# Kernel optimization log

Hardware: AMD Instinct MI355X
Metric: run time of the kernel (lower is better)

## Reference

```python
import jax, jax.numpy as jnp
import numpy as np

# Model config (matches init_kwargs)
DAG_DEPTH = 16
HIDDEN = 2048
B, T = 4, 4096
N = DAG_DEPTH                 # total_nodes
INIT_SLOTS = DAG_DEPTH // 2   # initial slots
INTER = DAG_DEPTH // 2        # intermediate slots / scan steps
LOG_CLAMP = 23.026
SIGN_TEMP = 1e-4


def _xavier(k, shape):
    fan_out, fan_in = shape
    lim = np.sqrt(6.0 / (fan_in + fan_out)).astype(np.float32)
    return jax.random.uniform(k, shape, jnp.float32, -lim, lim)


def setup_inputs() -> dict:
    key = jax.random.key(0)
    k0, k1, k2, k3 = jax.random.split(key, 4)
    return {
        "hidden": jax.random.normal(k0, (B, T, HIDDEN), jnp.float32),
        "W_init": _xavier(k1, (2 * N, HIDDEN)),
        "b_init": jnp.zeros((2 * N,), jnp.float32),
        "W_op": _xavier(k2, (INTER * N, HIDDEN)),
        "b_op": jnp.zeros((INTER * N,), jnp.float32),
        "W_gate": _xavier(k3, (INTER, HIDDEN)),
        "b_gate": jnp.zeros((INTER,), jnp.float32),
    }


def reference(hidden, W_init, b_init, W_op, b_op, W_gate, b_gate):
    Bb, Tt, H = hidden.shape
    # --- plan predictor ---
    init_raw = jnp.einsum('bth,oh->bto', hidden, W_init) + b_init        # (B,T,2N)
    V_mag = jnp.abs(init_raw[..., :N])                                   # (B,T,N)
    V_sign = jnp.tanh(init_raw[..., N:])                                 # (B,T,N)
    O = (jnp.einsum('bth,oh->bto', hidden, W_op) + b_op).reshape(Bb, Tt, INTER, N)
    G = jax.nn.sigmoid(jnp.einsum('bth,oh->bto', hidden, W_gate) + b_gate)  # (B,T,INTER)

    # --- sequential DAG execution (fixed INTER steps, vectorized over B,T) ---
    # NOTE: torch casts to float64 (float32 on mps); here we compute in float32,
    # identical math modulo precision (jax x64 is disabled by default).
    pos = jnp.arange(N)
    for step in range(INTER):
        valid = INIT_SLOTS + step
        mask = (pos < valid).astype(hidden.dtype)                        # causal mask over nodes
        O_s = O[:, :, step, :] * mask                                    # (B,T,N)
        G_s = G[:, :, step:step + 1]                                     # (B,T,1)
        signed = V_sign * V_mag
        log_mag = jnp.log(jnp.clip(V_mag, 1e-12))
        mixed = log_mag * (1.0 - G_s) + signed * G_s
        R = jnp.sum(O_s * mixed, axis=-1, keepdims=True)                 # (B,T,1)
        lin_sign = jnp.tanh(R / SIGN_TEMP)
        sign_prod = jnp.prod(V_sign * (jnp.abs(O_s) + 1.0), axis=-1, keepdims=True)
        log_sign = jnp.tanh(sign_prod / SIGN_TEMP)
        Vs_new = G_s * lin_sign + (1.0 - G_s) * log_sign
        Vm_new = G_s * jnp.abs(R) + (1.0 - G_s) * jnp.exp(jnp.clip(R, None, LOG_CLAMP))
        idx = INIT_SLOTS + step
        V_mag = V_mag.at[:, :, idx].set(Vm_new[..., 0])
        V_sign = V_sign.at[:, :, idx].set(Vs_new[..., 0])

    return V_sign[:, :, -1] * V_mag[:, :, -1]                            # (B,T)
```

## Files before the change

### kernel.cpp

```cpp
#include <hip/hip_runtime.h>
#include <math.h>

#define HID    2048
#define NROW   16384
#define NCOL   168
#define BM     64
#define KSTEPS 64
#define NSUP   32
#define NELEM  2112
#define SLICE  33792
#define SUPB   67584
#define CPD    172
#define NSLOT  16
#define NSTEP  8

typedef short short8 __attribute__((ext_vector_type(8)));
typedef float f32x4  __attribute__((ext_vector_type(4)));
typedef unsigned int u32x4 __attribute__((ext_vector_type(4)));

static __device__ __forceinline__ void wait_vm8() {
  asm volatile("s_waitcnt vmcnt(8)" ::: "memory");
}

static __device__ __forceinline__ unsigned pack_hi(unsigned u0, unsigned u1) {
  return __builtin_amdgcn_perm(u1, u0, 0x07060302u);
}

struct Planes { u32x4 p1, p2, p3; };
static __device__ __forceinline__ Planes split8(const float* x) {
  Planes P;
  #pragma unroll
  for (int q = 0; q < 4; ++q) {
    float x0 = x[2*q], x1 = x[2*q+1];
    unsigned u0 = __float_as_uint(x0), u1 = __float_as_uint(x1);
    P.p1[q] = pack_hi(u0, u1);
    float r0 = x0 - __uint_as_float(u0 & 0xFFFF0000u);
    float r1 = x1 - __uint_as_float(u1 & 0xFFFF0000u);
    unsigned v0 = __float_as_uint(r0), v1 = __float_as_uint(r1);
    P.p2[q] = pack_hi(v0, v1);
    float s0 = r0 - __uint_as_float(v0 & 0xFFFF0000u);
    float s1 = r1 - __uint_as_float(v1 & 0xFFFF0000u);
    P.p3[q] = pack_hi(__float_as_uint(s0), __float_as_uint(s1));
  }
  return P;
}

static __device__ __forceinline__ void loadA8(const float* p, float* x) {
  f32x4 a = *(const f32x4*)p;
  f32x4 b = *(const f32x4*)(p + 4);
  x[0]=a[0]; x[1]=a[1]; x[2]=a[2]; x[3]=a[3];
  x[4]=b[0]; x[5]=b[1]; x[6]=b[2]; x[7]=b[3];
}

static __device__ __forceinline__ f32x4 mf(short8 a, short8 b, f32x4 c) {
  return __builtin_amdgcn_mfma_f32_16x16x32_bf16(a, b, c, 0, 0, 0);
}

static __device__ __forceinline__ void gld_lds16(const void* g, void* l) {
  __builtin_amdgcn_global_load_lds(
      (const __attribute__((address_space(1))) unsigned int*)g,
      (__attribute__((address_space(3))) unsigned int*)l, 16, 0, 0);
}

__global__ void prep_b(const float* __restrict__ Wi, const float* __restrict__ Wo,
                       const float* __restrict__ Wg, u32x4* __restrict__ wsB) {
  int bid  = blockIdx.x;
  int kidx = bid / 11;
  int nt   = bid - kidx * 11;
  int l    = threadIdx.x;
  int col  = nt * 16 + (l & 15);
  int k0   = kidx * 32 + (l >> 4) * 8;

  float x[8];
  if (col < NCOL) {
    const float* wr = (col < 32)  ? (Wi + (size_t)col * HID)
                    : (col < 160) ? (Wo + (size_t)(col - 32) * HID)
                                  : (Wg + (size_t)(col - 160) * HID);
    loadA8(wr + k0, x);
  } else {
    #pragma unroll
    for (int i = 0; i < 8; ++i) x[i] = 0.f;
  }
  Planes P = split8(x);
  size_t base = (size_t)kidx * NELEM + (nt * 3) * 64 + l;
  wsB[base]       = P.p1;
  wsB[base + 64]  = P.p2;
  wsB[base + 128] = P.p3;
}

__global__ __launch_bounds__(512, 2)
void dag_main(const float* __restrict__ hidden, const u32x4* __restrict__ wsB,
              const float* __restrict__ b_init, const float* __restrict__ b_op,
              const float* __restrict__ b_gate, float* __restrict__ out)
{
  __shared__ __align__(16) char smem[2 * SUPB];

  const int tid = threadIdx.x;
  const int l   = tid & 63;
  const int w   = tid >> 6;
  const int wn  = w & 3;
  const int wm  = w >> 2;
  const int row0 = blockIdx.x * BM;
  const int r   = l & 15;
  const int kg  = l >> 4;

  const float* ap0 = hidden + (size_t)(row0 + wm * 32 + r) * HID + kg * 8;
  const float* ap1 = ap0 + (size_t)16 * HID;

  const int cb = 9 * wn + (wm ? ((wn == 3) ? 1 : 4) : 0);
  const u32x4* gsrc[5];
  char* ldst[5];
  #pragma unroll
  for (int i = 0; i < 5; ++i) {
    gsrc[i] = wsB + (size_t)(cb + i) * 64 + l;
    ldst[i] = smem + (cb + i) * 1024;
  }
  const char* brd0 = smem + (size_t)(9 * wn) * 1024 + (size_t)l * 16;

  f32x4 acc[2][3];
  const f32x4 zf = {0.f, 0.f, 0.f, 0.f};
  #pragma unroll
  for (int mt = 0; mt < 2; ++mt)
    #pragma unroll
    for (int j = 0; j < 3; ++j) acc[mt][j] = zf;

  float xe0[8], xe1[8], xo0[8], xo1[8];

#define STAGE(s_, sel_) do {                                                 \
    _Pragma("unroll")                                                        \
    for (int q = 0; q < 2; ++q)                                              \
      _Pragma("unroll")                                                      \
      for (int i = 0; i < 5; ++i)                                            \
        gld_lds16(gsrc[i] + (size_t)NELEM * (2 * (s_) + q),                  \
                  ldst[i] + (sel_) * SUPB + q * SLICE);                      \
  } while (0)

#define KSTEP(bb_, xc0_, xc1_, ISSA_, t2_) do {                              \
    short8 bf[9];                                                            \
    _Pragma("unroll")                                                        \
    for (int i = 0; i < 9; ++i)                                              \
      if (wn != 3 || i < 6) bf[i] = *(const short8*)((bb_) + i * 1024);      \
    Planes PA0 = split8(xc0_);                                               \
    Planes PA1 = split8(xc1_);                                               \
    if (ISSA_) {                                                             \
      loadA8(ap0 + (t2_) * 32, xc0_);                                        \
      loadA8(ap1 + (t2_) * 32, xc1_);                                        \
    }                                                                        \
    short8 a0p1 = __builtin_bit_cast(short8, PA0.p1);                        \
    short8 a0p2 = __builtin_bit_cast(short8, PA0.p2);                        \
    short8 a0p3 = __builtin_bit_cast(short8, PA0.p3);                        \
    short8 a1p1 = __builtin_bit_cast(short8, PA1.p1);                        \
    short8 a1p2 = __builtin_bit_cast(short8, PA1.p2);                        \
    short8 a1p3 = __builtin_bit_cast(short8, PA1.p3);                        \
    __builtin_amdgcn_s_setprio(1);                                           \
    _Pragma("unroll")                                                        \
    for (int j = 0; j < 3; ++j) {                                            \
      if (wn == 3 && j == 2) continue;                                       \
      short8 b1 = bf[j * 3 + 0];                                             \
      short8 b2 = bf[j * 3 + 1];                                             \
      short8 b3 = bf[j * 3 + 2];                                             \
      {                                                                      \
        f32x4 c = acc[0][j];                                                 \
        c = mf(a0p1, b1, c); c = mf(a0p1, b2, c); c = mf(a0p2, b1, c);       \
        c = mf(a0p1, b3, c); c = mf(a0p2, b2, c); c = mf(a0p3, b1, c);       \
        acc[0][j] = c;                                                       \
      }                                                                      \
      {                                                                      \
        f32x4 c = acc[1][j];                                                 \
        c = mf(a1p1, b1, c); c = mf(a1p1, b2, c); c = mf(a1p2, b1, c);       \
        c = mf(a1p1, b3, c); c = mf(a1p2, b2, c); c = mf(a1p3, b1, c);       \
        acc[1][j] = c;                                                       \
      }                                                                      \
    }                                                                        \
    __builtin_amdgcn_s_setprio(0);                                           \
  } while (0)

#define BODY(s_, p_, ISSUE_) do {                                            \
    wait_vm8();                                                              \
    __builtin_amdgcn_sched_barrier(0);                                       \
    __builtin_amdgcn_s_barrier();                                            \
    __builtin_amdgcn_sched_barrier(0);                                       \
    if (ISSUE_) STAGE((s_) + 1, (p_) ^ 1);                                   \
    const char* be = brd0 + (p_) * SUPB;                                     \
    KSTEP(be,         xe0, xe1, (ISSUE_), 2 * (s_) + 2);                     \
    KSTEP(be + SLICE, xo0, xo1, (ISSUE_), 2 * (s_) + 3);                     \
  } while (0)

  STAGE(0, 0);
  loadA8(ap0,      xe0);
  loadA8(ap1,      xe1);
  loadA8(ap0 + 32, xo0);
  loadA8(ap1 + 32, xo1);

  for (int s = 0; s < 30; s += 2) {
    BODY(s,     0, true);
    BODY(s + 1, 1, true);
  }
  BODY(30, 0, true);
  BODY(31, 1, false);
#undef BODY
#undef KSTEP
#undef STAGE

  __syncthreads();
  float (*sC)[CPD] = (float(*)[CPD])smem;
  #pragma unroll
  for (int mt = 0; mt < 2; ++mt) {
    #pragma unroll
    for (int j = 0; j < 3; ++j) {
      int col = wn * 48 + j * 16 + r;
      if (col < NCOL) {
        int row = wm * 32 + mt * 16 + kg * 4;
        sC[row + 0][col] = acc[mt][j][0];
        sC[row + 1][col] = acc[mt][j][1];
        sC[row + 2][col] = acc[mt][j][2];
        sC[row + 3][col] = acc[mt][j][3];
      }
    }
  }
  __syncthreads();

  if (tid < BM) {
    const int rr = tid;
    float Vm[NSLOT], Vs[NSLOT];
    #pragma unroll
    for (int i = 0; i < NSLOT; ++i) {
      float mv = sC[rr][i]      + b_init[i];
      float sv = sC[rr][16 + i] + b_init[16 + i];
      Vm[i] = fabsf(mv);
      Vs[i] = tanhf(sv);
    }
    float G[NSTEP];
    #pragma unroll
    for (int s = 0; s < NSTEP; ++s) {
      float gr = sC[rr][160 + s] + b_gate[s];
      G[s] = 1.0f / (1.0f + expf(-gr));
    }
    #pragma unroll
    for (int s = 0; s < NSTEP; ++s) {
      const float g = G[s];
      float R = 0.f, sp = 1.f;
      #pragma unroll
      for (int i = 0; i < NSLOT; ++i) {
        float Osi = (i < 8 + s) ? (sC[rr][32 + s * 16 + i] + b_op[s * 16 + i]) : 0.f;
        float sgn   = Vs[i] * Vm[i];
        float logm  = logf(fmaxf(Vm[i], 1e-12f));
        float mixed = logm * (1.f - g) + sgn * g;
        R  += Osi * mixed;
        sp *= Vs[i] * (fabsf(Osi) + 1.f);
      }
      float lin_sign = tanhf(R  / 1e-4f);
      float log_sign = tanhf(sp / 1e-4f);
      float vs_new = g * lin_sign + (1.f - g) * log_sign;
      float vm_new = g * fabsf(R) + (1.f - g) * expf(fminf(R, 23.026f));
      Vm[8 + s] = vm_new;
      Vs[8 + s] = vs_new;
    }
    out[row0 + rr] = Vs[NSLOT - 1] * Vm[NSLOT - 1];
  }
}

extern "C" void kernel_launch(void* const* d_in, const int* in_sizes, int n_in,
                              void* d_out, int out_size, void* d_ws, size_t ws_size,
                              hipStream_t stream) {
  (void)in_sizes; (void)n_in; (void)out_size; (void)ws_size;
  const float* hidden = (const float*)d_in[0];
  const float* W_init = (const float*)d_in[1];
  const float* b_init = (const float*)d_in[2];
  const float* W_op   = (const float*)d_in[3];
  const float* b_op   = (const float*)d_in[4];
  const float* W_gate = (const float*)d_in[5];
  const float* b_gate = (const float*)d_in[6];
  float* out = (float*)d_out;
  u32x4* wsB = (u32x4*)d_ws;

  prep_b<<<dim3(704), dim3(64), 0, stream>>>(W_init, W_op, W_gate, wsB);
  dag_main<<<dim3(NROW / BM), dim3(512), 0, stream>>>(hidden, wsB, b_init, b_op,
                                                      b_gate, out);
}
```

Before: 100.5 us.

## Split GEMM warp tiles to 16 rows per wave with 1024-thread blocks

Doubles the block to 16 waves, so each wave computes a 16-row by 48-column tile instead of 32 rows. The staging of B into LDS is redistributed across the four row-groups of waves, with 2-3 chunks each, and the vmcnt wait threshold is lowered to match the fewer loads per thread. The goal is more waves in flight to hide latency and lower register pressure per wave. Each B fragment read from LDS is now reused for only one A tile, so LDS read traffic doubles per MFMA, and occupancy drops to one block per CU.

```diff
diff --git a/kernel.cpp b/kernel.cpp
--- a/kernel.cpp
+++ b/kernel.cpp
@@ -6,7 +6,6 @@
 #define NCOL   168
 #define BM     64
 #define KSTEPS 64
-#define NSUP   32
 #define NELEM  2112
 #define SLICE  33792
 #define SUPB   67584
@@ -18,8 +17,8 @@
 typedef float f32x4  __attribute__((ext_vector_type(4)));
 typedef unsigned int u32x4 __attribute__((ext_vector_type(4)));
 
-static __device__ __forceinline__ void wait_vm8() {
-  asm volatile("s_waitcnt vmcnt(8)" ::: "memory");
+static __device__ __forceinline__ void wait_vm4() {
+  asm volatile("s_waitcnt vmcnt(4)" ::: "memory");
 }
 
 static __device__ __forceinline__ unsigned pack_hi(unsigned u0, unsigned u1) {
@@ -88,7 +87,7 @@
   wsB[base + 128] = P.p3;
 }
 
-__global__ __launch_bounds__(512, 2)
+__global__ __launch_bounds__(1024, 1)
 void dag_main(const float* __restrict__ hidden, const u32x4* __restrict__ wsB,
               const float* __restrict__ b_init, const float* __restrict__ b_op,
               const float* __restrict__ b_gate, float* __restrict__ out)
@@ -104,93 +103,74 @@
   const int r   = l & 15;
   const int kg  = l >> 4;
 
-  const float* ap0 = hidden + (size_t)(row0 + wm * 32 + r) * HID + kg * 8;
-  const float* ap1 = ap0 + (size_t)16 * HID;
-
-  const int cb = 9 * wn + (wm ? ((wn == 3) ? 1 : 4) : 0);
-  const u32x4* gsrc[5];
-  char* ldst[5];
-  #pragma unroll
-  for (int i = 0; i < 5; ++i) {
-    gsrc[i] = wsB + (size_t)(cb + i) * 64 + l;
-    ldst[i] = smem + (cb + i) * 1024;
+  const float* ap = hidden + (size_t)(row0 + wm * 16 + r) * HID + kg * 8;
+
+  const int D  = (wm == 0) ? 3 : 2;
+  const int s0 = (wm == 0) ? 0 : 2 * wm + 1;
+  const u32x4* gsrc[3];
+  char* ldst[3];
+  #pragma unroll
+  for (int i = 0; i < 3; ++i) {
+    int ci = s0 + i; if (ci > 8) ci = 8;
+    int cp = (wn == 3 && ci >= 6) ? ci - 6 : ci;
+    int c  = 9 * wn + cp;
+    gsrc[i] = wsB + (size_t)c * 64 + l;
+    ldst[i] = smem + c * 1024;
   }
   const char* brd0 = smem + (size_t)(9 * wn) * 1024 + (size_t)l * 16;
 
-  f32x4 acc[2][3];
+  f32x4 acc[3];
   const f32x4 zf = {0.f, 0.f, 0.f, 0.f};
   #pragma unroll
-  for (int mt = 0; mt < 2; ++mt)
-    #pragma unroll
-    for (int j = 0; j < 3; ++j) acc[mt][j] = zf;
-
-  float xe0[8], xe1[8], xo0[8], xo1[8];
+  for (int j = 0; j < 3; ++j) acc[j] = zf;
+
+  float xe[8], xo[8];
 
 #define STAGE(s_, sel_) do {                                                 \
     _Pragma("unroll")                                                        \
     for (int q = 0; q < 2; ++q)                                              \
       _Pragma("unroll")                                                      \
-      for (int i = 0; i < 5; ++i)                                            \
-        gld_lds16(gsrc[i] + (size_t)NELEM * (2 * (s_) + q),                  \
-                  ldst[i] + (sel_) * SUPB + q * SLICE);                      \
+      for (int i = 0; i < 3; ++i)                                            \
+        if (i < D)                                                           \
+          gld_lds16(gsrc[i] + (size_t)NELEM * (2 * (s_) + q),                \
+                    ldst[i] + (sel_) * SUPB + q * SLICE);                    \
   } while (0)
 
-#define KSTEP(bb_, xc0_, xc1_, ISSA_, t2_) do {                              \
-    short8 bf[9];                                                            \
-    _Pragma("unroll")                                                        \
-    for (int i = 0; i < 9; ++i)                                              \
-      if (wn != 3 || i < 6) bf[i] = *(const short8*)((bb_) + i * 1024);      \
-    Planes PA0 = split8(xc0_);                                               \
-    Planes PA1 = split8(xc1_);                                               \
-    if (ISSA_) {                                                             \
-      loadA8(ap0 + (t2_) * 32, xc0_);                                        \
-      loadA8(ap1 + (t2_) * 32, xc1_);                                        \
-    }                                                                        \
-    short8 a0p1 = __builtin_bit_cast(short8, PA0.p1);                        \
-    short8 a0p2 = __builtin_bit_cast(short8, PA0.p2);                        \
-    short8 a0p3 = __builtin_bit_cast(short8, PA0.p3);                        \
-    short8 a1p1 = __builtin_bit_cast(short8, PA1.p1);                        \
-    short8 a1p2 = __builtin_bit_cast(short8, PA1.p2);                        \
-    short8 a1p3 = __builtin_bit_cast(short8, PA1.p3);                        \
+#define KSTEP(bb_, xc_, ISSA_, t2_) do {                                     \
+    Planes PA = split8(xc_);                                                 \
+    if (ISSA_) loadA8(ap + (t2_) * 32, xc_);                                 \
+    short8 ap1 = __builtin_bit_cast(short8, PA.p1);                          \
+    short8 ap2 = __builtin_bit_cast(short8, PA.p2);                          \
+    short8 ap3 = __builtin_bit_cast(short8, PA.p3);                          \
     __builtin_amdgcn_s_setprio(1);                                           \
     _Pragma("unroll")                                                        \
     for (int j = 0; j < 3; ++j) {                                            \
       if (wn == 3 && j == 2) continue;                                       \
-      short8 b1 = bf[j * 3 + 0];                                             \
-      short8 b2 = bf[j * 3 + 1];                                             \
-      short8 b3 = bf[j * 3 + 2];                                             \
-      {                                                                      \
-        f32x4 c = acc[0][j];                                                 \
-        c = mf(a0p1, b1, c); c = mf(a0p1, b2, c); c = mf(a0p2, b1, c);       \
-        c = mf(a0p1, b3, c); c = mf(a0p2, b2, c); c = mf(a0p3, b1, c);       \
-        acc[0][j] = c;                                                       \
-      }                                                                      \
-      {                                                                      \
-        f32x4 c = acc[1][j];                                                 \
-        c = mf(a1p1, b1, c); c = mf(a1p1, b2, c); c = mf(a1p2, b1, c);       \
-        c = mf(a1p1, b3, c); c = mf(a1p2, b2, c); c = mf(a1p3, b1, c);       \
-        acc[1][j] = c;                                                       \
-      }                                                                      \
+      short8 b1 = *(const short8*)((bb_) + (j * 3 + 0) * 1024);              \
+      short8 b2 = *(const short8*)((bb_) + (j * 3 + 1) * 1024);              \
+      short8 b3 = *(const short8*)((bb_) + (j * 3 + 2) * 1024);              \
+      f32x4 c = acc[j];                                                      \
+      c = mf(ap1, b1, c); c = mf(ap1, b2, c); c = mf(ap2, b1, c);            \
+      c = mf(ap1, b3, c); c = mf(ap2, b2, c); c = mf(ap3, b1, c);            \
+      acc[j] = c;                                                            \
     }                                                                        \
     __builtin_amdgcn_s_setprio(0);                                           \
   } while (0)
 
 #define BODY(s_, p_, ISSUE_) do {                                            \
-    wait_vm8();                                                              \
+    wait_vm4();                                                              \
     __builtin_amdgcn_sched_barrier(0);                                       \
     __builtin_amdgcn_s_barrier();                                            \
     __builtin_amdgcn_sched_barrier(0);                                       \
     if (ISSUE_) STAGE((s_) + 1, (p_) ^ 1);                                   \
     const char* be = brd0 + (p_) * SUPB;                                     \
-    KSTEP(be,         xe0, xe1, (ISSUE_), 2 * (s_) + 2);                     \
-    KSTEP(be + SLICE, xo0, xo1, (ISSUE_), 2 * (s_) + 3);                     \
+    KSTEP(be,         xe, (ISSUE_), 2 * (s_) + 2);                           \
+    KSTEP(be + SLICE, xo, (ISSUE_), 2 * (s_) + 3);                           \
   } while (0)
 
   STAGE(0, 0);
-  loadA8(ap0,      xe0);
-  loadA8(ap1,      xe1);
-  loadA8(ap0 + 32, xo0);
-  loadA8(ap1 + 32, xo1);
+  loadA8(ap,      xe);
+  loadA8(ap + 32, xo);
 
   for (int s = 0; s < 30; s += 2) {
     BODY(s,     0, true);
@@ -205,17 +185,14 @@
   __syncthreads();
   float (*sC)[CPD] = (float(*)[CPD])smem;
   #pragma unroll
-  for (int mt = 0; mt < 2; ++mt) {
-    #pragma unroll
-    for (int j = 0; j < 3; ++j) {
-      int col = wn * 48 + j * 16 + r;
-      if (col < NCOL) {
-        int row = wm * 32 + mt * 16 + kg * 4;
-        sC[row + 0][col] = acc[mt][j][0];
-        sC[row + 1][col] = acc[mt][j][1];
-        sC[row + 2][col] = acc[mt][j][2];
-        sC[row + 3][col] = acc[mt][j][3];
-      }
+  for (int j = 0; j < 3; ++j) {
+    int col = wn * 48 + j * 16 + r;
+    if (col < NCOL) {
+      int row = wm * 16 + kg * 4;
+      sC[row + 0][col] = acc[j][0];
+      sC[row + 1][col] = acc[j][1];
+      sC[row + 2][col] = acc[j][2];
+      sC[row + 3][col] = acc[j][3];
     }
   }
   __syncthreads();
@@ -275,6 +252,6 @@
   u32x4* wsB = (u32x4*)d_ws;
 
   prep_b<<<dim3(704), dim3(64), 0, stream>>>(W_init, W_op, W_gate, wsB);
-  dag_main<<<dim3(NROW / BM), dim3(512), 0, stream>>>(hidden, wsB, b_init, b_op,
-                                                      b_gate, out);
-}
+  dag_main<<<dim3(NROW / BM), dim3(1024), 0, stream>>>(hidden, wsB, b_init, b_op,
+                                                       b_gate, out);
+}
```

Measured after the change: 100.1 us. About the same (-0.3%).
